# Optimization experiments

Measured on AMD Instinct MI355X. Metric: run time of the kernel, lower is better.

## Reference

```python
import jax, jax.numpy as jnp
import numpy as np

B, S, D, H = 2, 2048, 1024, 16
HD = D // H  # head_dim = 64


def setup_inputs() -> dict:
    key = jax.random.key(0)
    ks = jax.random.split(key, 6)
    scale = 0.02
    return {
        "x": jax.random.normal(ks[0], (B, S, D), dtype=jnp.float32),
        "wq": jax.random.normal(ks[1], (D, D), dtype=jnp.float32) * scale,  # torch Linear weight [out,in]
        "wk": jax.random.normal(ks[2], (D, D), dtype=jnp.float32) * scale,
        "wv": jax.random.normal(ks[3], (D, D), dtype=jnp.float32) * scale,
        "wo": jax.random.normal(ks[4], (D, D), dtype=jnp.float32) * scale,
        "bo": jnp.zeros((D,), dtype=jnp.float32),
    }


def reference(x, wq, wk, wv, wo, bo):
    b, t, d = x.shape
    # projections (torch nn.Linear: x @ W.T), split into heads -> [b, h, t, hd]
    def split_heads(y):
        return y.reshape(b, t, H, HD).transpose(0, 2, 1, 3)

    q = split_heads(x @ wq.T)
    k = split_heads(x @ wk.T)
    v = split_heads(x @ wv.T)

    scores = jnp.einsum("bhqd,bhkd->bhqk", q, k)  # [b,h,t,t]
    causal = jnp.triu(jnp.ones((t, t), dtype=bool), k=1)
    scores = jnp.where(causal, -jnp.inf, scores)
    attn = jax.nn.softmax(scores / jnp.sqrt(jnp.asarray(HD, scores.dtype)), axis=-1)
    # dropout p=0.0 -> identity (eval-mode reference)
    ctx = jnp.einsum("bhqk,bhkd->bhqd", attn, v)
    ctx = ctx.transpose(0, 2, 1, 3).reshape(b, t, d)
    return ctx @ wo.T + bo
```

## Files before the change

kernel.cpp:

```cpp
#include <hip/hip_runtime.h>
#include <hip/hip_bf16.h>
#include <stdint.h>
#include <math.h>

#define NH   16
#define HDIM 64
#define SEQ  2048
#define DM   1024
#define NB   2
#define MTOK (NB * SEQ)

typedef __bf16 bf16x8 __attribute__((ext_vector_type(8)));
typedef __bf16 bf16x4 __attribute__((ext_vector_type(4)));
typedef short  short4v __attribute__((ext_vector_type(4)));
typedef float  f32x4  __attribute__((ext_vector_type(4)));

__device__ __forceinline__ unsigned short f2bf(float f) {
  union { float f; unsigned int u; } c; c.f = f;
  unsigned int u = c.u;
  return (unsigned short)((u + 0x7FFFu + ((u >> 16) & 1u)) >> 16);
}
__device__ __forceinline__ float bf2f(unsigned short s) {
  union { unsigned int u; float f; } c; c.u = ((unsigned int)s) << 16;
  return c.f;
}
__device__ __forceinline__ unsigned int pk2bf(float a, float b) {
  __hip_bfloat162 h = __float22bfloat162_rn(float2{a, b});
  return *reinterpret_cast<unsigned int*>(&h);
}

__device__ __forceinline__ float fexp2(float x) {
#if __has_builtin(__builtin_amdgcn_exp2f)
  return __builtin_amdgcn_exp2f(x);
#else
  return exp2f(x);
#endif
}

__device__ __forceinline__ f32x4 mfma16(short4v a, short4v b, f32x4 c) {
#if __has_builtin(__builtin_amdgcn_mfma_f32_16x16x16_bf16)
  return __builtin_amdgcn_mfma_f32_16x16x16_bf16(
      __builtin_bit_cast(bf16x4, a), __builtin_bit_cast(bf16x4, b), c, 0, 0, 0);
#else
  return __builtin_amdgcn_mfma_f32_16x16x16bf16_1k(a, b, c, 0, 0, 0);
#endif
}

__device__ __forceinline__ void async_copy16(const void* g, void* l) {
  __builtin_amdgcn_global_load_lds((__attribute__((address_space(1))) void*)g,
                                   (__attribute__((address_space(3))) void*)l,
                                   16, 0, 0);
}

__global__ void cast_all(const float* __restrict__ x,  const float* __restrict__ wq,
                         const float* __restrict__ wk, const float* __restrict__ wv,
                         const float* __restrict__ wo,
                         unsigned short* __restrict__ xb,
                         unsigned short* __restrict__ wqkvb,
                         unsigned short* __restrict__ wob) {
  const int i = blockIdx.x * 256 + threadIdx.x;
  float4 v;
  uint2* dstp;
  int idx;
  if (i < (1 << 20)) {
    v = reinterpret_cast<const float4*>(x)[i];
    dstp = reinterpret_cast<uint2*>(xb); idx = i;
  } else {
    const int j = i - (1 << 20);
    const int seg = j >> 18;
    idx = j & ((1 << 18) - 1);
    const float* w = (seg == 0) ? wq : (seg == 1) ? wk : (seg == 2) ? wv : wo;
    v = reinterpret_cast<const float4*>(w)[idx];
    if (seg < 3) { dstp = reinterpret_cast<uint2*>(wqkvb); idx += seg * (1 << 18); }
    else         { dstp = reinterpret_cast<uint2*>(wob); }
  }
  uint2 o;
  o.x = pk2bf(v.x, v.y); o.y = pk2bf(v.z, v.w);
  dstp[idx] = o;
}

#define QSCALE 0.1803368801111244f
template <int MODE>
__global__ __launch_bounds__(256, 3) void gemm_bt(
    const unsigned short* __restrict__ A,
    const unsigned short* __restrict__ B,
    unsigned short* __restrict__ qo, unsigned short* __restrict__ ko,
    unsigned short* __restrict__ vo,
    float* __restrict__ co, const float* __restrict__ bias,
    int M, int N, int K) {
  constexpr int BN = (MODE == 0) ? 128 : 64;
  constexpr int TJ = BN / 32;
  constexpr int RB = BN * 4 / 256;
  __shared__ __align__(16) unsigned short As[128 * 32];
  __shared__ __align__(16) unsigned short Bs[BN * 32];

  const int tid  = threadIdx.x;
  const int lane = tid & 63;
  const int wave = tid >> 6;
  const int l15  = lane & 15;
  const int quad = lane >> 4;
  const int wm   = (wave >> 1) * 64;
  const int wn   = (wave & 1) * (BN / 2);
  const int m0   = blockIdx.x * 128;
  const int n0   = blockIdx.y * BN;

  f32x4 acc[4][TJ];
#pragma unroll
  for (int a = 0; a < 4; ++a)
#pragma unroll
    for (int b = 0; b < TJ; ++b) acc[a][b] = f32x4{0.f, 0.f, 0.f, 0.f};

  for (int k0 = 0; k0 < K; k0 += 32) {
    __syncthreads();
#pragma unroll
    for (int s = 0; s < 2; ++s) {
      const int c   = tid + s * 256;
      const int row = c >> 2;
      const int col = (c & 3) * 8;
      unsigned short* lA = As + ((size_t)wave * 64 + s * 256) * 8;
      async_copy16(A + (size_t)(m0 + row) * K + k0 + col, lA);
    }
#pragma unroll
    for (int s = 0; s < RB; ++s) {
      const int c   = tid + s * 256;
      const int row = c >> 2;
      const int col = (c & 3) * 8;
      unsigned short* lB = Bs + ((size_t)wave * 64 + s * 256) * 8;
      async_copy16(B + (size_t)(n0 + row) * K + k0 + col, lB);
    }
    __syncthreads();

    bf16x8 af[4], bfr[TJ];
#pragma unroll
    for (int t = 0; t < 4; ++t)
      af[t]  = *reinterpret_cast<const bf16x8*>(As + (wm + t * 16 + l15) * 32 + quad * 8);
#pragma unroll
    for (int t = 0; t < TJ; ++t)
      bfr[t] = *reinterpret_cast<const bf16x8*>(Bs + (wn + t * 16 + l15) * 32 + quad * 8);
#pragma unroll
    for (int ti = 0; ti < 4; ++ti)
#pragma unroll
      for (int tj = 0; tj < TJ; ++tj)
        acc[ti][tj] = __builtin_amdgcn_mfma_f32_16x16x32_bf16(af[ti], bfr[tj], acc[ti][tj], 0, 0, 0);
  }

#pragma unroll
  for (int ti = 0; ti < 4; ++ti) {
#pragma unroll
    for (int tj = 0; tj < TJ; ++tj) {
      const int mb = m0 + wm + ti * 16 + quad * 4;
      const int n  = n0 + wn + tj * 16 + l15;
      if (MODE == 0) {
        const int which = n >> 10;
        const int n1 = n & 1023;
        const int h = n1 >> 6, d = n1 & 63;
        const int b = mb >> 11, s = mb & 2047;
        if (which == 0) {
          const size_t idx = ((size_t)(b * NH + h) * SEQ + s) * HDIM + d;
#pragma unroll
          for (int r = 0; r < 4; ++r) qo[idx + (size_t)r * HDIM] = f2bf(acc[ti][tj][r] * QSCALE);
        } else if (which == 1) {
          const size_t idx = ((size_t)(b * NH + h) * SEQ + s) * HDIM + d;
#pragma unroll
          for (int r = 0; r < 4; ++r) ko[idx + (size_t)r * HDIM] = f2bf(acc[ti][tj][r]);
        } else {
          const size_t idx = ((size_t)(b * NH + h) * HDIM + d) * SEQ + s;
          uint2 pk;
          pk.x = pk2bf(acc[ti][tj][0], acc[ti][tj][1]);
          pk.y = pk2bf(acc[ti][tj][2], acc[ti][tj][3]);
          *reinterpret_cast<uint2*>(vo + idx) = pk;
        }
      } else {
#pragma unroll
        for (int r = 0; r < 4; ++r)
          co[(size_t)(mb + r) * N + n] = acc[ti][tj][r] + bias[n];
      }
    }
  }
}

#define KST 72

__global__ __launch_bounds__(256, 8) void flash_attn_mfma(
    const unsigned short* __restrict__ Qb,
    const unsigned short* __restrict__ Kb,
    const unsigned short* __restrict__ Vtg,
    unsigned short* __restrict__ ctx,
    unsigned short* __restrict__ pO,
    float* __restrict__ pL) {
  __shared__ __align__(16) unsigned short Ks[64 * KST];
  __shared__ __align__(16) unsigned short Vt[64 * KST];

  const int tid  = threadIdx.x;
  const int bh   = blockIdx.y;
  const int lane = tid & 63;
  const int wave = tid >> 6;
  const int l15  = lane & 15;
  const int quad = lane >> 4;

  int qt, chunk, nch;
  {
    const int x = blockIdx.x;
    if (x < 12)      { qt = x;                 chunk = 0;            nch = 1; }
    else if (x < 36) { qt = 12 + (x - 12) / 2; chunk = (x - 12) % 2; nch = 2; }
    else             { qt = 24 + (x - 36) / 3; chunk = (x - 36) % 3; nch = 3; }
  }
  const int q0 = qt * 64;
  const int c0 = chunk * 12;
  const int c1 = min(qt, c0 + 11);

  const size_t baseQK = (size_t)bh * SEQ * HDIM;
  const size_t baseV  = (size_t)bh * HDIM * SEQ;

  const int srow = tid >> 3;
  const int scol = (tid & 7) * 8;

  bf16x8 qf[2];
  {
    const unsigned short* qp = Qb + baseQK + (size_t)(q0 + wave * 16 + l15) * HDIM + quad * 8;
    qf[0] = *reinterpret_cast<const bf16x8*>(qp);
    qf[1] = *reinterpret_cast<const bf16x8*>(qp + 32);
  }

  float l_acc = 0.f;
  f32x4 o[4];
#pragma unroll
  for (int td = 0; td < 4; ++td) o[td] = f32x4{0.f, 0.f, 0.f, 0.f};

  for (int kt = c0; kt <= c1; ++kt) {
    __syncthreads();
    {
      const uint4 k0v = *reinterpret_cast<const uint4*>(Kb + baseQK + (size_t)(kt * 64 + srow) * HDIM + scol);
      const uint4 k1v = *reinterpret_cast<const uint4*>(Kb + baseQK + (size_t)(kt * 64 + srow + 32) * HDIM + scol);
      const uint4 v0v = *reinterpret_cast<const uint4*>(Vtg + baseV + (size_t)srow * SEQ + kt * 64 + scol);
      const uint4 v1v = *reinterpret_cast<const uint4*>(Vtg + baseV + (size_t)(srow + 32) * SEQ + kt * 64 + scol);
      *reinterpret_cast<uint4*>(&Ks[srow * KST + scol]) = k0v;
      *reinterpret_cast<uint4*>(&Ks[(srow + 32) * KST + scol]) = k1v;
      *reinterpret_cast<uint4*>(&Vt[srow * KST + scol]) = v0v;
      *reinterpret_cast<uint4*>(&Vt[(srow + 32) * KST + scol]) = v1v;
    }
    __syncthreads();

    const int tmax = (kt == qt) ? wave : 3;

#pragma unroll
    for (int t = 0; t < 4; ++t) {
      if (t <= tmax) {
        f32x4 c = f32x4{0.f, 0.f, 0.f, 0.f};
        const int krow = (t * 16 + l15) * KST;
        const bf16x8 kf0 = *reinterpret_cast<const bf16x8*>(&Ks[krow + quad * 8]);
        const bf16x8 kf1 = *reinterpret_cast<const bf16x8*>(&Ks[krow + 32 + quad * 8]);
        c = __builtin_amdgcn_mfma_f32_16x16x32_bf16(kf0, qf[0], c, 0, 0, 0);
        c = __builtin_amdgcn_mfma_f32_16x16x32_bf16(kf1, qf[1], c, 0, 0, 0);
        if (kt == qt && t == wave) {
#pragma unroll
          for (int r = 0; r < 4; ++r)
            if (quad * 4 + r > l15) c[r] = -INFINITY;
        }

        const float p0 = fexp2(c[0]);
        const float p1 = fexp2(c[1]);
        const float p2 = fexp2(c[2]);
        const float p3 = fexp2(c[3]);
        l_acc += (p0 + p1) + (p2 + p3);
        union { uint2 u; short4v s; } pf;
        pf.u.x = pk2bf(p0, p1);
        pf.u.y = pk2bf(p2, p3);

#pragma unroll
        for (int td = 0; td < 4; ++td) {
          const short4v vf = *reinterpret_cast<const short4v*>(
              &Vt[(td * 16 + l15) * KST + t * 16 + quad * 4]);
          o[td] = mfma16(pf.s, vf, o[td]);
        }
      }
    }
  }

  float l_s = l_acc;
  l_s += __shfl_xor(l_s, 16, 64);
  l_s += __shfl_xor(l_s, 32, 64);

  if (nch == 1) {
    const float linv = 1.f / l_s;
    const int b = bh >> 4, h = bh & 15;
#pragma unroll
    for (int r = 0; r < 4; ++r) {
      const float lr = __shfl(linv, quad * 4 + r, 64);
      const int sr = q0 + wave * 16 + quad * 4 + r;
      const size_t ob = (size_t)(b * SEQ + sr) * DM + h * HDIM + l15;
#pragma unroll
      for (int td = 0; td < 4; ++td)
        ctx[ob + td * 16] = f2bf(o[td][r] * lr);
    }
  } else {
    const int pb = (qt < 24) ? 2 * (qt - 12) : 24 + 3 * (qt - 24);
    const int pidx = bh * 48 + pb + chunk;
    if (quad == 0) pL[pidx * 64 + wave * 16 + l15] = l_s;
    unsigned short* po = pO + (size_t)pidx * 4096;
#pragma unroll
    for (int r = 0; r < 4; ++r) {
      const int ql = wave * 16 + quad * 4 + r;
#pragma unroll
      for (int td = 0; td < 4; ++td)
        po[ql * 64 + td * 16 + l15] = f2bf(o[td][r]);
    }
  }
}

__global__ __launch_bounds__(256, 8) void attn_reduce(
    const unsigned short* __restrict__ pO, const float* __restrict__ pL,
    unsigned short* __restrict__ ctx) {
  const int x = blockIdx.x;
  int qt, pb, nch;
  if (x < 12) { qt = 12 + x; pb = 2 * x;            nch = 2; }
  else        { qt = 24 + (x - 12); pb = 24 + 3 * (x - 12); nch = 3; }
  const int bh = blockIdx.y;
  const int b = bh >> 4, h = bh & 15;
  const int pidx = bh * 48 + pb;

  const int tid = threadIdx.x;
  const int ql  = tid >> 2;
  const int d0  = (tid & 3) * 16;

  float acc[16];
#pragma unroll
  for (int e = 0; e < 16; ++e) acc[e] = 0.f;
  float lsum = 0.f;

  for (int c = 0; c < nch; ++c) {
    lsum += pL[(pidx + c) * 64 + ql];
    const unsigned short* src = pO + (size_t)(pidx + c) * 4096 + ql * 64 + d0;
    const uint4 v0 = *reinterpret_cast<const uint4*>(src);
    const uint4 v1 = *reinterpret_cast<const uint4*>(src + 8);
    const unsigned short* u = reinterpret_cast<const unsigned short*>(&v0);
    const unsigned short* w = reinterpret_cast<const unsigned short*>(&v1);
#pragma unroll
    for (int e = 0; e < 8; ++e) { acc[e] += bf2f(u[e]); acc[8 + e] += bf2f(w[e]); }
  }

  const float linv = 1.f / lsum;
  unsigned int outw[8];
#pragma unroll
  for (int e = 0; e < 8; ++e)
    outw[e] = pk2bf(acc[2 * e] * linv, acc[2 * e + 1] * linv);
  unsigned short* dst = ctx + (size_t)(b * SEQ + qt * 64 + ql) * DM + h * HDIM + d0;
  *reinterpret_cast<uint4*>(dst)     = *reinterpret_cast<uint4*>(&outw[0]);
  *reinterpret_cast<uint4*>(dst + 8) = *reinterpret_cast<uint4*>(&outw[4]);
}

extern "C" void kernel_launch(void* const* d_in, const int* in_sizes, int n_in,
                              void* d_out, int out_size, void* d_ws, size_t ws_size,
                              hipStream_t stream) {
  const float* x  = (const float*)d_in[0];
  const float* wq = (const float*)d_in[1];
  const float* wk = (const float*)d_in[2];
  const float* wv = (const float*)d_in[3];
  const float* wo = (const float*)d_in[4];
  const float* bo = (const float*)d_in[5];
  float* out = (float*)d_out;

  char* ws = (char*)d_ws;
  unsigned short* xb    = (unsigned short*)(ws);
  unsigned short* wqkvb = (unsigned short*)(ws + (8ull  << 20));
  unsigned short* wob   = (unsigned short*)(ws + (14ull << 20));
  unsigned short* Qb    = (unsigned short*)(ws + (16ull << 20));
  unsigned short* Kb    = (unsigned short*)(ws + (24ull << 20));
  unsigned short* Vtg   = (unsigned short*)(ws + (32ull << 20));
  unsigned short* ctxb  = (unsigned short*)(ws + (40ull << 20));
  unsigned short* pO    = (unsigned short*)(ws);
  float*          pL    = (float*)(ws + (12ull << 20));

  cast_all<<<8192, 256, 0, stream>>>(x, wq, wk, wv, wo, xb, wqkvb, wob);

  dim3 g1(MTOK / 128, (3 * DM) / 128);
  gemm_bt<0><<<g1, 256, 0, stream>>>(xb, wqkvb, Qb, Kb, Vtg, nullptr, nullptr,
                                     MTOK, 3 * DM, DM);

  dim3 g2(60, NB * NH);
  flash_attn_mfma<<<g2, 256, 0, stream>>>(Qb, Kb, Vtg, ctxb, pO, pL);

  dim3 gr(20, NB * NH);
  attn_reduce<<<gr, 256, 0, stream>>>(pO, pL, ctxb);

  dim3 g3(MTOK / 128, DM / 64);
  gemm_bt<1><<<g3, 256, 0, stream>>>(ctxb, wob, nullptr, nullptr, nullptr, out, bo,
                                     MTOK, DM, DM);
}
```

Before: 190.2 us.

## Process 128 query rows per attention block to reuse K/V tiles

The flash attention kernel now gives each block a 128-row query tile, handled as two 64-row sub-tiles per wave. Each K/V tile staged in shared memory serves twice as many queries, which halves global K/V traffic and barrier count per query. The causal chunking, the partial-output layout, the reduce kernel indexing and the pL offset are all remapped to match. Occupancy hints drop (8 to 4 for attention, 3 to 2 for the GEMM), which gives more registers per thread but leaves fewer resident waves and fewer attention blocks to balance the causal workload.

New measurement: 182.8 us. 1.04x faster.

```diff
diff --git a/kernel.cpp b/kernel.cpp
--- a/kernel.cpp
+++ b/kernel.cpp
@@ -81,7 +81,7 @@
 
 #define QSCALE 0.1803368801111244f
 template <int MODE>
-__global__ __launch_bounds__(256, 3) void gemm_bt(
+__global__ __launch_bounds__(256, 2) void gemm_bt(
     const unsigned short* __restrict__ A,
     const unsigned short* __restrict__ B,
     unsigned short* __restrict__ qo, unsigned short* __restrict__ ko,
@@ -181,7 +181,7 @@
 
 #define KST 72
 
-__global__ __launch_bounds__(256, 8) void flash_attn_mfma(
+__global__ __launch_bounds__(256, 4) void flash_attn_mfma(
     const unsigned short* __restrict__ Qb,
     const unsigned short* __restrict__ Kb,
     const unsigned short* __restrict__ Vtg,
@@ -201,13 +201,14 @@
   int qt, chunk, nch;
   {
     const int x = blockIdx.x;
-    if (x < 12)      { qt = x;                 chunk = 0;            nch = 1; }
-    else if (x < 36) { qt = 12 + (x - 12) / 2; chunk = (x - 12) % 2; nch = 2; }
-    else             { qt = 24 + (x - 36) / 3; chunk = (x - 36) % 3; nch = 3; }
-  }
-  const int q0 = qt * 64;
-  const int c0 = chunk * 12;
-  const int c1 = min(qt, c0 + 11);
+    if (x < 6)       { qt = x;                chunk = 0;            nch = 1; }
+    else if (x < 18) { qt = 6 + (x - 6) / 2;  chunk = (x - 6) % 2;  nch = 2; }
+    else             { qt = 12 + (x - 18) / 3; chunk = (x - 18) % 3; nch = 3; }
+  }
+  const int q0   = qt * 128;
+  const int kmax = 2 * qt + 1;
+  const int c0   = chunk * 12;
+  const int c1   = min(kmax, c0 + 11);
 
   const size_t baseQK = (size_t)bh * SEQ * HDIM;
   const size_t baseV  = (size_t)bh * HDIM * SEQ;
@@ -215,17 +216,21 @@
   const int srow = tid >> 3;
   const int scol = (tid & 7) * 8;
 
-  bf16x8 qf[2];
-  {
-    const unsigned short* qp = Qb + baseQK + (size_t)(q0 + wave * 16 + l15) * HDIM + quad * 8;
-    qf[0] = *reinterpret_cast<const bf16x8*>(qp);
-    qf[1] = *reinterpret_cast<const bf16x8*>(qp + 32);
-  }
-
-  float l_acc = 0.f;
-  f32x4 o[4];
-#pragma unroll
-  for (int td = 0; td < 4; ++td) o[td] = f32x4{0.f, 0.f, 0.f, 0.f};
+  bf16x8 qf[2][2];
+#pragma unroll
+  for (int sp = 0; sp < 2; ++sp) {
+    const unsigned short* qp =
+        Qb + baseQK + (size_t)(q0 + sp * 64 + wave * 16 + l15) * HDIM + quad * 8;
+    qf[sp][0] = *reinterpret_cast<const bf16x8*>(qp);
+    qf[sp][1] = *reinterpret_cast<const bf16x8*>(qp + 32);
+  }
+
+  float l_acc[2] = {0.f, 0.f};
+  f32x4 o[2][4];
+#pragma unroll
+  for (int sp = 0; sp < 2; ++sp)
+#pragma unroll
+    for (int td = 0; td < 4; ++td) o[sp][td] = f32x4{0.f, 0.f, 0.f, 0.f};
 
   for (int kt = c0; kt <= c1; ++kt) {
     __syncthreads();
@@ -241,69 +246,88 @@
     }
     __syncthreads();
 
-    const int tmax = (kt == qt) ? wave : 3;
+    const int rel0 = 8 * qt + wave - 4 * kt;
+    const int rel1 = rel0 + 4;
 
 #pragma unroll
     for (int t = 0; t < 4; ++t) {
-      if (t <= tmax) {
-        f32x4 c = f32x4{0.f, 0.f, 0.f, 0.f};
+      if (t <= rel1) {
         const int krow = (t * 16 + l15) * KST;
         const bf16x8 kf0 = *reinterpret_cast<const bf16x8*>(&Ks[krow + quad * 8]);
         const bf16x8 kf1 = *reinterpret_cast<const bf16x8*>(&Ks[krow + 32 + quad * 8]);
-        c = __builtin_amdgcn_mfma_f32_16x16x32_bf16(kf0, qf[0], c, 0, 0, 0);
-        c = __builtin_amdgcn_mfma_f32_16x16x32_bf16(kf1, qf[1], c, 0, 0, 0);
-        if (kt == qt && t == wave) {
-#pragma unroll
-          for (int r = 0; r < 4; ++r)
-            if (quad * 4 + r > l15) c[r] = -INFINITY;
-        }
-
-        const float p0 = fexp2(c[0]);
-        const float p1 = fexp2(c[1]);
-        const float p2 = fexp2(c[2]);
-        const float p3 = fexp2(c[3]);
-        l_acc += (p0 + p1) + (p2 + p3);
-        union { uint2 u; short4v s; } pf;
-        pf.u.x = pk2bf(p0, p1);
-        pf.u.y = pk2bf(p2, p3);
-
-#pragma unroll
-        for (int td = 0; td < 4; ++td) {
-          const short4v vf = *reinterpret_cast<const short4v*>(
-              &Vt[(td * 16 + l15) * KST + t * 16 + quad * 4]);
-          o[td] = mfma16(pf.s, vf, o[td]);
+
+#pragma unroll
+        for (int sp = 0; sp < 2; ++sp) {
+          const int rel = sp ? rel1 : rel0;
+          if (t <= rel) {
+            f32x4 c = f32x4{0.f, 0.f, 0.f, 0.f};
+            c = __builtin_amdgcn_mfma_f32_16x16x32_bf16(kf0, qf[sp][0], c, 0, 0, 0);
+            c = __builtin_amdgcn_mfma_f32_16x16x32_bf16(kf1, qf[sp][1], c, 0, 0, 0);
+            if (t == rel) {
+#pragma unroll
+              for (int r = 0; r < 4; ++r)
+                if (quad * 4 + r > l15) c[r] = -INFINITY;
+            }
+
+            const float p0 = fexp2(c[0]);
+            const float p1 = fexp2(c[1]);
+            const float p2 = fexp2(c[2]);
+            const float p3 = fexp2(c[3]);
+            l_acc[sp] += (p0 + p1) + (p2 + p3);
+            union { uint2 u; short4v s; } pf;
+            pf.u.x = pk2bf(p0, p1);
+            pf.u.y = pk2bf(p2, p3);
+
+#pragma unroll
+            for (int td = 0; td < 4; ++td) {
+              const short4v vf = *reinterpret_cast<const short4v*>(
+                  &Vt[(td * 16 + l15) * KST + t * 16 + quad * 4]);
+              o[sp][td] = mfma16(pf.s, vf, o[sp][td]);
+            }
+          }
         }
       }
     }
   }
 
-  float l_s = l_acc;
-  l_s += __shfl_xor(l_s, 16, 64);
-  l_s += __shfl_xor(l_s, 32, 64);
+  float l_s[2];
+#pragma unroll
+  for (int sp = 0; sp < 2; ++sp) {
+    float v = l_acc[sp];
+    v += __shfl_xor(v, 16, 64);
+    v += __shfl_xor(v, 32, 64);
+    l_s[sp] = v;
+  }
 
   if (nch == 1) {
-    const float linv = 1.f / l_s;
     const int b = bh >> 4, h = bh & 15;
 #pragma unroll
-    for (int r = 0; r < 4; ++r) {
-      const float lr = __shfl(linv, quad * 4 + r, 64);
-      const int sr = q0 + wave * 16 + quad * 4 + r;
-      const size_t ob = (size_t)(b * SEQ + sr) * DM + h * HDIM + l15;
-#pragma unroll
-      for (int td = 0; td < 4; ++td)
-        ctx[ob + td * 16] = f2bf(o[td][r] * lr);
+    for (int sp = 0; sp < 2; ++sp) {
+      const float linv = 1.f / l_s[sp];
+#pragma unroll
+      for (int r = 0; r < 4; ++r) {
+        const float lr = __shfl(linv, quad * 4 + r, 64);
+        const int sr = q0 + sp * 64 + wave * 16 + quad * 4 + r;
+        const size_t ob = (size_t)(b * SEQ + sr) * DM + h * HDIM + l15;
+#pragma unroll
+        for (int td = 0; td < 4; ++td)
+          ctx[ob + td * 16] = f2bf(o[sp][td][r] * lr);
+      }
     }
   } else {
-    const int pb = (qt < 24) ? 2 * (qt - 12) : 24 + 3 * (qt - 24);
-    const int pidx = bh * 48 + pb + chunk;
-    if (quad == 0) pL[pidx * 64 + wave * 16 + l15] = l_s;
-    unsigned short* po = pO + (size_t)pidx * 4096;
-#pragma unroll
-    for (int r = 0; r < 4; ++r) {
-      const int ql = wave * 16 + quad * 4 + r;
-#pragma unroll
-      for (int td = 0; td < 4; ++td)
-        po[ql * 64 + td * 16 + l15] = f2bf(o[td][r]);
+    const int pb = (qt < 12) ? 2 * (qt - 6) : 12 + 3 * (qt - 12);
+    const int pidx = bh * 24 + pb + chunk;
+    unsigned short* po = pO + (size_t)pidx * 8192;
+#pragma unroll
+    for (int sp = 0; sp < 2; ++sp) {
+      if (quad == 0) pL[pidx * 128 + sp * 64 + wave * 16 + l15] = l_s[sp];
+#pragma unroll
+      for (int r = 0; r < 4; ++r) {
+        const int ql = sp * 64 + wave * 16 + quad * 4 + r;
+#pragma unroll
+        for (int td = 0; td < 4; ++td)
+          po[ql * 64 + td * 16 + l15] = f2bf(o[sp][td][r]);
+      }
     }
   }
 }
@@ -311,16 +335,18 @@
 __global__ __launch_bounds__(256, 8) void attn_reduce(
     const unsigned short* __restrict__ pO, const float* __restrict__ pL,
     unsigned short* __restrict__ ctx) {
-  const int x = blockIdx.x;
+  const int x    = blockIdx.x;
+  const int pair = x >> 1;
+  const int half = x & 1;
   int qt, pb, nch;
-  if (x < 12) { qt = 12 + x; pb = 2 * x;            nch = 2; }
-  else        { qt = 24 + (x - 12); pb = 24 + 3 * (x - 12); nch = 3; }
+  if (pair < 6) { qt = 6 + pair;          pb = 2 * pair;            nch = 2; }
+  else          { qt = 12 + (pair - 6);   pb = 12 + 3 * (pair - 6); nch = 3; }
   const int bh = blockIdx.y;
   const int b = bh >> 4, h = bh & 15;
-  const int pidx = bh * 48 + pb;
+  const int pidx = bh * 24 + pb;
 
   const int tid = threadIdx.x;
-  const int ql  = tid >> 2;
+  const int ql  = half * 64 + (tid >> 2);
   const int d0  = (tid & 3) * 16;
 
   float acc[16];
@@ -329,8 +355,8 @@
   float lsum = 0.f;
 
   for (int c = 0; c < nch; ++c) {
-    lsum += pL[(pidx + c) * 64 + ql];
-    const unsigned short* src = pO + (size_t)(pidx + c) * 4096 + ql * 64 + d0;
+    lsum += pL[(pidx + c) * 128 + ql];
+    const unsigned short* src = pO + (size_t)(pidx + c) * 8192 + ql * 64 + d0;
     const uint4 v0 = *reinterpret_cast<const uint4*>(src);
     const uint4 v1 = *reinterpret_cast<const uint4*>(src + 8);
     const unsigned short* u = reinterpret_cast<const unsigned short*>(&v0);
@@ -344,7 +370,7 @@
 #pragma unroll
   for (int e = 0; e < 8; ++e)
     outw[e] = pk2bf(acc[2 * e] * linv, acc[2 * e + 1] * linv);
-  unsigned short* dst = ctx + (size_t)(b * SEQ + qt * 64 + ql) * DM + h * HDIM + d0;
+  unsigned short* dst = ctx + (size_t)(b * SEQ + qt * 128 + ql) * DM + h * HDIM + d0;
   *reinterpret_cast<uint4*>(dst)     = *reinterpret_cast<uint4*>(&outw[0]);
   *reinterpret_cast<uint4*>(dst + 8) = *reinterpret_cast<uint4*>(&outw[4]);
 }
@@ -369,7 +395,7 @@
   unsigned short* Vtg   = (unsigned short*)(ws + (32ull << 20));
   unsigned short* ctxb  = (unsigned short*)(ws + (40ull << 20));
   unsigned short* pO    = (unsigned short*)(ws);
-  float*          pL    = (float*)(ws + (12ull << 20));
+  float*          pL    = (float*)(ws + (12ull << 20) + (512ull << 10));
 
   cast_all<<<8192, 256, 0, stream>>>(x, wq, wk, wv, wo, xb, wqkvb, wob);
 
@@ -377,7 +403,7 @@
   gemm_bt<0><<<g1, 256, 0, stream>>>(xb, wqkvb, Qb, Kb, Vtg, nullptr, nullptr,
                                      MTOK, 3 * DM, DM);
 
-  dim3 g2(60, NB * NH);
+  dim3 g2(30, NB * NH);
   flash_attn_mfma<<<g2, 256, 0, stream>>>(Qb, Kb, Vtg, ctxb, pO, pL);
 
   dim3 gr(20, NB * NH);
```
